# Kernel optimization log

Measured on AMD Instinct MI355X. Metric: run time of the kernel, lower is better.

The kernel has to match this reference:

```python
import jax, jax.numpy as jnp
import numpy as np

LORA_SCALE = 1.0 / 4.0  # alpha=1, rank=4
TAU_IOU = 0.1


def lora(x, W, A, B):
    # x @ W.T + (x @ A.T) @ B.T * scaling
    return x @ W.T + (x @ A.T) @ B.T * LORA_SCALE


def decode(h, Wd1, bd1, Wd2, bd2):
    # mask_decoder: Linear(embed,64) -> ReLU -> Linear(64,1)
    return (jax.nn.relu(h @ Wd1.T + bd1) @ Wd2.T + bd2)[..., 0]


def setup_inputs() -> dict:
    key = jax.random.key(0)
    ks = jax.random.split(key, 16)
    B, N, I, E, R = 2, 8192, 32, 128, 4
    s = lambda k, shape, f=0.05: jax.random.normal(k, shape, dtype=jnp.float32) * f
    return {
        "points": jax.random.normal(ks[0], (B, N, 3), dtype=jnp.float32),
        "pos_coords": jax.random.normal(ks[1], (B, I, 3), dtype=jnp.float32),
        "W1": s(ks[2], (64, 3), 0.3),
        "A1": s(ks[3], (R, 3), 0.3),
        "B1": s(ks[4], (64, R), 0.3),
        "W2": s(ks[5], (E, 64), 0.1),
        "A2": s(ks[6], (R, 64), 0.1),
        "B2": s(ks[7], (E, R), 0.1),
        "Wp": s(ks[8], (E, 3), 0.3),
        "bp": s(ks[9], (E,), 0.1),
        "Wd1": s(ks[10], (64, E), 0.1),
        "bd1": s(ks[11], (64,), 0.1),
        "Wd2": s(ks[12], (1, 64), 0.1),
        "bd2": s(ks[13], (1,), 0.1),
    }


def npc_neg_coords(initial_logits, pos_coords, key):
    # Vectorized replacement of the double python loop: for each (b,i),
    # uniformly sample one j with iou[b,i,j] >= tau (Gumbel-max trick);
    # if none, leave zeros.
    B, I, N = initial_logits.shape
    masks = (jax.nn.sigmoid(initial_logits) > 0.5).astype(initial_logits.dtype)  # [B,I,N]
    inter = jnp.einsum("bin,bjn->bij", masks, masks)
    m_sum = masks.sum(axis=2)  # [B,I]
    union = m_sum[:, :, None] + m_sum[:, None, :] - inter
    iou = inter / (union + 1e-6)
    iou = iou * (1.0 - jnp.eye(I, dtype=iou.dtype))  # zero diagonal
    cand = iou >= TAU_IOU  # [B,I,I]
    gumbel = -jnp.log(-jnp.log(jax.random.uniform(key, cand.shape, minval=1e-20, maxval=1.0)))
    scores = jnp.where(cand, gumbel, -jnp.inf)
    idx = jnp.argmax(scores, axis=-1)  # [B,I]
    valid = cand.any(axis=-1)  # [B,I]
    picked = jnp.take_along_axis(pos_coords, idx[..., None], axis=1)  # [B,I,3]
    return jnp.where(valid[..., None], picked, 0.0)


def reference(points, pos_coords, W1, A1, B1, W2, A2, B2, Wp, bp, Wd1, bd1, Wd2, bd2):
    # encoder: LoRA(3->64) -> ReLU -> LoRA(64->128)
    point_feats = lora(jax.nn.relu(lora(points, W1, A1, B1)), W2, A2, B2)  # [B,N,E]
    pos_embed = pos_coords @ Wp.T + bp  # [B,I,E]
    # [B,I,N,E] combined features
    initial_logits = decode(point_feats[:, None, :, :] + pos_embed[:, :, None, :], Wd1, bd1, Wd2, bd2)  # [B,I,N]
    neg_coords = npc_neg_coords(initial_logits, pos_coords, jax.random.key(42))
    neg_embed = neg_coords @ Wp.T + bp  # [B,I,E]
    refined_logits = decode(
        point_feats[:, None, :, :] + (pos_embed - neg_embed)[:, :, None, :], Wd1, bd1, Wd2, bd2
    )  # [B,I,N]
    return refined_logits, point_feats
```

## Files before the change

kernel.cpp:

```cpp
#include <hip/hip_runtime.h>

#define B_  2
#define N_  8192
#define I_  32
#define E_  128
#define H_  64
#define BN_ (B_*N_)
#define NW_ (N_/64)

typedef unsigned long long u64;

__device__ float g_pe  [B_*I_*E_];
__device__ float g_v1  [B_*I_*H_];
__device__ float g_v2  [B_*I_*H_];
__device__ float g_wd1t[E_*H_];
__device__ float g_u   [H_*BN_];
__device__ u64   g_masks[B_*I_*NW_];
__device__ int   g_inter[B_*I_*I_];

__device__ __forceinline__ unsigned rotl_(unsigned x, unsigned n){ return (x<<n)|(x>>(32u-n)); }

__device__ void threefry_42(unsigned x0, unsigned x1, unsigned* r0, unsigned* r1){
  const unsigned ks0 = 0u, ks1 = 42u, ks2 = 0x1BD11BDAu ^ 0u ^ 42u;
  x0 += ks0; x1 += ks1;
  x0+=x1; x1=rotl_(x1,13); x1^=x0;
  x0+=x1; x1=rotl_(x1,15); x1^=x0;
  x0+=x1; x1=rotl_(x1,26); x1^=x0;
  x0+=x1; x1=rotl_(x1, 6); x1^=x0;
  x0+=ks1; x1+=ks2+1u;
  x0+=x1; x1=rotl_(x1,17); x1^=x0;
  x0+=x1; x1=rotl_(x1,29); x1^=x0;
  x0+=x1; x1=rotl_(x1,16); x1^=x0;
  x0+=x1; x1=rotl_(x1,24); x1^=x0;
  x0+=ks2; x1+=ks0+2u;
  x0+=x1; x1=rotl_(x1,13); x1^=x0;
  x0+=x1; x1=rotl_(x1,15); x1^=x0;
  x0+=x1; x1=rotl_(x1,26); x1^=x0;
  x0+=x1; x1=rotl_(x1, 6); x1^=x0;
  x0+=ks0; x1+=ks1+3u;
  x0+=x1; x1=rotl_(x1,17); x1^=x0;
  x0+=x1; x1=rotl_(x1,29); x1^=x0;
  x0+=x1; x1=rotl_(x1,16); x1^=x0;
  x0+=x1; x1=rotl_(x1,24); x1^=x0;
  x0+=ks1; x1+=ks2+4u;
  x0+=x1; x1=rotl_(x1,13); x1^=x0;
  x0+=x1; x1=rotl_(x1,15); x1^=x0;
  x0+=x1; x1=rotl_(x1,26); x1^=x0;
  x0+=x1; x1=rotl_(x1, 6); x1^=x0;
  x0+=ks2; x1+=ks0+5u;
  *r0 = x0; *r1 = x1;
}

__device__ float jax_uniform_2048(int e){
  unsigned o0, o1;
  threefry_42(0u, (unsigned)e, &o0, &o1);
  unsigned bits = o0 ^ o1;
  float u = __uint_as_float((bits >> 9) | 0x3f800000u) - 1.0f;
  u = u + 1e-20f;
  return fmaxf(1e-20f, u);
}

__global__ void __launch_bounds__(256) prep_kernel(
    const float* __restrict__ pos_coords,
    const float* __restrict__ Wp, const float* __restrict__ bp,
    const float* __restrict__ Wd1,const float* __restrict__ bd1)
{
  __shared__ float t_l [E_*65];
  __shared__ float pe_l[E_];
  const int row = blockIdx.x;
  const int tid = threadIdx.x;

  for (int idx = tid; idx < H_*E_; idx += 256){
    int k = idx >> 7, e = idx & 127;
    t_l[e*65 + k] = Wd1[idx];
  }
  if (tid < E_){
    const int e = tid;
    float s = pos_coords[row*3+0] * Wp[e*3+0];
    s = fmaf(pos_coords[row*3+1], Wp[e*3+1], s);
    s = fmaf(pos_coords[row*3+2], Wp[e*3+2], s);
    const float pe = s + bp[e];
    g_pe[row*E_ + e] = pe;
    pe_l[e] = pe;
  }
  __syncthreads();

  if (row == 0){
    for (int idx = tid; idx < E_*H_; idx += 256){
      int e = idx >> 6, k = idx & 63;
      g_wd1t[idx] = t_l[e*65 + k];
    }
  }
  if (tid < H_){
    const int k = tid;
    float s = 0.f;
    for (int e = 0; e < 128; ++e)
      s = fmaf(pe_l[e], t_l[e*65 + k], s);
    g_v1[row*H_ + k] = s + bd1[k];
  }
}

__global__ void __launch_bounds__(512) enc_kernel(
    const float* __restrict__ points,
    const float* __restrict__ W1, const float* __restrict__ A1,
    const float* __restrict__ B1, const float* __restrict__ W2,
    const float* __restrict__ A2, const float* __restrict__ B2,
    const float* __restrict__ Wd2,const float* __restrict__ bd2,
    float* __restrict__ out_pf)
{
  __shared__ float pf_l[E_*65];
  __shared__ float u_l [64*65];
  const int tid  = threadIdx.x;
  const int w_u  = __builtin_amdgcn_readfirstlane(tid >> 6);
  const int lane = tid & 63;
  const int p0   = blockIdx.x * 64;
  const int p    = p0 + lane;
  const int b    = blockIdx.x >> 7;

  const float x0 = points[p*3+0];
  const float x1 = points[p*3+1];
  const float x2 = points[p*3+2];

  float a1[4];
  #pragma unroll
  for (int r = 0; r < 4; ++r){
    float s = x0 * A1[r*3+0];
    s = fmaf(x1, A1[r*3+1], s);
    s = fmaf(x2, A1[r*3+2], s);
    a1[r] = s;
  }
  float t1[64];
  #pragma unroll
  for (int k = 0; k < 64; ++k){
    float s = x0 * W1[k*3+0];
    s = fmaf(x1, W1[k*3+1], s);
    s = fmaf(x2, W1[k*3+2], s);
    float l = a1[0] * B1[k*4+0];
    l = fmaf(a1[1], B1[k*4+1], l);
    l = fmaf(a1[2], B1[k*4+2], l);
    l = fmaf(a1[3], B1[k*4+3], l);
    t1[k] = fmaxf(fmaf(0.25f, l, s), 0.0f);
  }
  float a2[4];
  #pragma unroll
  for (int r = 0; r < 4; ++r){
    float s = 0.f;
    #pragma unroll
    for (int j = 0; j < 64; ++j) s = fmaf(t1[j], A2[r*64+j], s);
    a2[r] = s;
  }

  const int e0 = w_u * 16;
  for (int ei = 0; ei < 16; ++ei){
    const int e = e0 + ei;
    float s1 = 0.f;
    #pragma unroll
    for (int j = 0; j < 64; ++j) s1 = fmaf(t1[j], W2[e*64+j], s1);
    float s2 = a2[0] * B2[e*4+0];
    s2 = fmaf(a2[1], B2[e*4+1], s2);
    s2 = fmaf(a2[2], B2[e*4+2], s2);
    s2 = fmaf(a2[3], B2[e*4+3], s2);
    pf_l[e*65 + lane] = fmaf(0.25f, s2, s1);
  }
  __syncthreads();

  const int kbase = w_u * 8;
  float uacc[8];
  #pragma unroll
  for (int kk = 0; kk < 8; ++kk) uacc[kk] = 0.f;
  for (int e = 0; e < 128; ++e){
    const float pf = pf_l[e*65 + lane];
    #pragma unroll
    for (int kk = 0; kk < 8; ++kk)
      uacc[kk] = fmaf(pf, g_wd1t[e*64 + kbase + kk], uacc[kk]);
  }
  #pragma unroll
  for (int kk = 0; kk < 8; ++kk){
    g_u[(size_t)(kbase + kk) * BN_ + p] = uacc[kk];
    u_l[lane*65 + kbase + kk] = uacc[kk];
  }
  __syncthreads();

  for (int idx = tid; idx < 64*E_; idx += 512){
    const int pt = idx >> 7, e = idx & 127;
    out_pf[(size_t)p0 * E_ + idx] = pf_l[e*65 + pt];
  }

  const float bd2v = bd2[0];
  float acc[4];
  #pragma unroll
  for (int ii = 0; ii < 4; ++ii) acc[ii] = 0.f;
  const int ibase = w_u * 4;
  const float* v = g_v1 + ((b * I_ + ibase) << 6);
  for (int k = 0; k < 64; ++k){
    const float wd2k = Wd2[k];
    const float uk = u_l[lane*65 + k];
    #pragma unroll
    for (int ii = 0; ii < 4; ++ii)
      acc[ii] = fmaf(wd2k, fmaxf(uk + v[ii*64 + k], 0.0f), acc[ii]);
  }
  #pragma unroll
  for (int ii = 0; ii < 4; ++ii){
    const int i = ibase + ii;
    u64 bal = __ballot(acc[ii] + bd2v > 0.0f);
    if (lane == 0) g_masks[(size_t)(b * I_ + i) * NW_ + (blockIdx.x & 127)] = bal;
  }
}

__global__ void __launch_bounds__(256) inter_kernel()
{
  const int r   = blockIdx.x;
  const int b   = r >> 5;
  const int tid = threadIdx.x;
  const int j   = tid >> 3;
  const int ws  = (tid & 7) * 16;
  const u64* mi = g_masks + (size_t)r * NW_;
  const u64* mj = g_masks + (size_t)(b*32 + j) * NW_;
  int s = 0;
  #pragma unroll
  for (int w = 0; w < 16; ++w)
    s += __popcll(mi[ws + w] & mj[ws + w]);
  s += __shfl_xor(s, 1, 64);
  s += __shfl_xor(s, 2, 64);
  s += __shfl_xor(s, 4, 64);
  if ((tid & 7) == 0) g_inter[r*32 + j] = s;
}

__global__ void __launch_bounds__(256) sample_kernel(
    const float* __restrict__ pos_coords,
    const float* __restrict__ Wp, const float* __restrict__ bp,
    const float* __restrict__ bd1)
{
  __shared__ int   inter_l[2048];
  __shared__ float delta_l[4*E_];
  __shared__ float nc_l[4][3];
  const int tid  = threadIdx.x;
  const int row0 = blockIdx.x * 4;

  for (int idx = tid; idx < 2048; idx += 256) inter_l[idx] = g_inter[idx];
  __syncthreads();

  if (tid < 4){
    const int row = row0 + tid;
    const int b = row >> 5;
    const int i = row & 31;
    const int msum_i = inter_l[(b << 10) + (i << 5) + i];
    float best = -INFINITY; int bestj = 0; bool any = false;
    for (int j = 0; j < 32; ++j){
      const int inter = inter_l[(b << 10) + (i << 5) + j];
      const int msum_j = inter_l[(b << 10) + (j << 5) + j];
      const int uni   = msum_i + msum_j - inter;
      const float iou = (float)inter / ((float)uni + 1e-6f);
      const bool cand = (j != i) && (iou >= 0.1f);
      if (cand){
        any = true;
        const float uu = jax_uniform_2048((row << 5) + j);
        const float g  = -logf(-logf(uu));
        if (g > best){ best = g; bestj = j; }
      }
    }
    nc_l[tid][0] = any ? pos_coords[(b*32 + bestj)*3 + 0] : 0.f;
    nc_l[tid][1] = any ? pos_coords[(b*32 + bestj)*3 + 1] : 0.f;
    nc_l[tid][2] = any ? pos_coords[(b*32 + bestj)*3 + 2] : 0.f;
  }
  __syncthreads();

  for (int idx = tid; idx < 4*E_; idx += 256){
    const int rl = idx >> 7, e = idx & 127;
    float ne = nc_l[rl][0] * Wp[e*3+0];
    ne = fmaf(nc_l[rl][1], Wp[e*3+1], ne);
    ne = fmaf(nc_l[rl][2], Wp[e*3+2], ne);
    ne = ne + bp[e];
    delta_l[idx] = g_pe[(row0 + rl)*E_ + e] - ne;
  }
  __syncthreads();

  {
    const int rl = tid >> 6, k = tid & 63;
    float s = 0.f;
    for (int e = 0; e < 128; ++e)
      s = fmaf(delta_l[rl*E_ + e], g_wd1t[e*64 + k], s);
    g_v2[(row0 + rl)*H_ + k] = s + bd1[k];
  }
}

__global__ void __launch_bounds__(256) dec_kernel(
    const float* __restrict__ Wd2, const float* __restrict__ bd2,
    float* __restrict__ out0)
{
  const int tid  = threadIdx.x;
  const int w_u  = __builtin_amdgcn_readfirstlane(tid >> 6);
  const int lane = tid & 63;
  const int bc   = blockIdx.x;
  const int b    = bc >> 8;
  const int nb   = (bc & 127) << 6;
  const int ih   = (bc >> 7) & 1;
  const int n    = nb + lane;
  const int p    = b * N_ + n;

  float u[64];
  #pragma unroll
  for (int k = 0; k < 64; ++k) u[k] = g_u[(size_t)k * BN_ + p];

  const float bd2v = bd2[0];
  float acc[4];
  #pragma unroll
  for (int ii = 0; ii < 4; ++ii) acc[ii] = 0.f;
  const int ibase = ih * 16 + w_u * 4;
  const float* v = g_v2 + ((b * I_ + ibase) << 6);
  for (int k = 0; k < 64; ++k){
    const float wd2k = Wd2[k];
    const float uk = u[k];
    #pragma unroll
    for (int ii = 0; ii < 4; ++ii)
      acc[ii] = fmaf(wd2k, fmaxf(uk + v[ii*64 + k], 0.0f), acc[ii]);
  }
  #pragma unroll
  for (int ii = 0; ii < 4; ++ii){
    const int i = ibase + ii;
    out0[(size_t)(b * I_ + i) * N_ + n] = acc[ii] + bd2v;
  }
}

extern "C" void kernel_launch(void* const* d_in, const int* in_sizes, int n_in,
                              void* d_out, int out_size, void* d_ws, size_t ws_size,
                              hipStream_t stream)
{
  (void)in_sizes; (void)n_in; (void)out_size; (void)d_ws; (void)ws_size;
  const float* points     = (const float*)d_in[0];
  const float* pos_coords = (const float*)d_in[1];
  const float* W1  = (const float*)d_in[2];
  const float* A1  = (const float*)d_in[3];
  const float* B1  = (const float*)d_in[4];
  const float* W2  = (const float*)d_in[5];
  const float* A2  = (const float*)d_in[6];
  const float* B2  = (const float*)d_in[7];
  const float* Wp  = (const float*)d_in[8];
  const float* bp  = (const float*)d_in[9];
  const float* Wd1 = (const float*)d_in[10];
  const float* bd1 = (const float*)d_in[11];
  const float* Wd2 = (const float*)d_in[12];
  const float* bd2 = (const float*)d_in[13];

  float* out0   = (float*)d_out;
  float* out_pf = out0 + (size_t)B_ * I_ * N_;

  prep_kernel<<<64, 256, 0, stream>>>(pos_coords, Wp, bp, Wd1, bd1);
  enc_kernel<<<256, 512, 0, stream>>>(points, W1, A1, B1, W2, A2, B2,
                                      Wd2, bd2, out_pf);
  inter_kernel<<<64, 256, 0, stream>>>();
  sample_kernel<<<16, 256, 0, stream>>>(pos_coords, Wp, bp, bd1);
  dec_kernel<<<512, 256, 0, stream>>>(Wd2, bd2, out0);
}
```

Before: 149.8 us.

## Double block size in encoder and decoder, stage u vectors through LDS

The encoder kernel goes from 512 to 1024 threads per block, so each wave computes half as many embedding channels, hidden units and instance masks. The decoder now launches 256 blocks of 1024 threads. Each block loads its 64-point u tile into shared memory once and shares it across all 32 instances, instead of every thread holding 64 registers loaded from global memory twice per point. The goal is more waves in flight and less redundant global reading of u, at the cost of larger blocks, an extra barrier and LDS reads in the inner loop.

```diff
diff --git a/kernel.cpp b/kernel.cpp
--- a/kernel.cpp
+++ b/kernel.cpp
@@ -100,7 +100,7 @@
   }
 }
 
-__global__ void __launch_bounds__(512) enc_kernel(
+__global__ void __launch_bounds__(1024) enc_kernel(
     const float* __restrict__ points,
     const float* __restrict__ W1, const float* __restrict__ A1,
     const float* __restrict__ B1, const float* __restrict__ W2,
@@ -150,8 +150,8 @@
     a2[r] = s;
   }
 
-  const int e0 = w_u * 16;
-  for (int ei = 0; ei < 16; ++ei){
+  const int e0 = w_u * 8;
+  for (int ei = 0; ei < 8; ++ei){
     const int e = e0 + ei;
     float s1 = 0.f;
     #pragma unroll
@@ -164,43 +164,41 @@
   }
   __syncthreads();
 
-  const int kbase = w_u * 8;
-  float uacc[8];
-  #pragma unroll
-  for (int kk = 0; kk < 8; ++kk) uacc[kk] = 0.f;
+  const int kbase = w_u * 4;
+  float uacc[4];
+  #pragma unroll
+  for (int kk = 0; kk < 4; ++kk) uacc[kk] = 0.f;
   for (int e = 0; e < 128; ++e){
     const float pf = pf_l[e*65 + lane];
     #pragma unroll
-    for (int kk = 0; kk < 8; ++kk)
+    for (int kk = 0; kk < 4; ++kk)
       uacc[kk] = fmaf(pf, g_wd1t[e*64 + kbase + kk], uacc[kk]);
   }
   #pragma unroll
-  for (int kk = 0; kk < 8; ++kk){
+  for (int kk = 0; kk < 4; ++kk){
     g_u[(size_t)(kbase + kk) * BN_ + p] = uacc[kk];
     u_l[lane*65 + kbase + kk] = uacc[kk];
   }
   __syncthreads();
 
-  for (int idx = tid; idx < 64*E_; idx += 512){
+  for (int idx = tid; idx < 64*E_; idx += 1024){
     const int pt = idx >> 7, e = idx & 127;
     out_pf[(size_t)p0 * E_ + idx] = pf_l[e*65 + pt];
   }
 
   const float bd2v = bd2[0];
-  float acc[4];
-  #pragma unroll
-  for (int ii = 0; ii < 4; ++ii) acc[ii] = 0.f;
-  const int ibase = w_u * 4;
+  float acc[2];
+  acc[0] = 0.f; acc[1] = 0.f;
+  const int ibase = w_u * 2;
   const float* v = g_v1 + ((b * I_ + ibase) << 6);
   for (int k = 0; k < 64; ++k){
     const float wd2k = Wd2[k];
     const float uk = u_l[lane*65 + k];
-    #pragma unroll
-    for (int ii = 0; ii < 4; ++ii)
-      acc[ii] = fmaf(wd2k, fmaxf(uk + v[ii*64 + k], 0.0f), acc[ii]);
-  }
-  #pragma unroll
-  for (int ii = 0; ii < 4; ++ii){
+    acc[0] = fmaf(wd2k, fmaxf(uk + v[k],      0.0f), acc[0]);
+    acc[1] = fmaf(wd2k, fmaxf(uk + v[64 + k], 0.0f), acc[1]);
+  }
+  #pragma unroll
+  for (int ii = 0; ii < 2; ++ii){
     const int i = ibase + ii;
     u64 bal = __ballot(acc[ii] + bd2v > 0.0f);
     if (lane == 0) g_masks[(size_t)(b * I_ + i) * NW_ + (blockIdx.x & 127)] = bal;
@@ -284,39 +282,38 @@
   }
 }
 
-__global__ void __launch_bounds__(256) dec_kernel(
+__global__ void __launch_bounds__(1024) dec_kernel(
     const float* __restrict__ Wd2, const float* __restrict__ bd2,
     float* __restrict__ out0)
 {
+  __shared__ float u_l[64*65];
   const int tid  = threadIdx.x;
   const int w_u  = __builtin_amdgcn_readfirstlane(tid >> 6);
   const int lane = tid & 63;
   const int bc   = blockIdx.x;
-  const int b    = bc >> 8;
+  const int b    = bc >> 7;
   const int nb   = (bc & 127) << 6;
-  const int ih   = (bc >> 7) & 1;
   const int n    = nb + lane;
-  const int p    = b * N_ + n;
-
-  float u[64];
-  #pragma unroll
-  for (int k = 0; k < 64; ++k) u[k] = g_u[(size_t)k * BN_ + p];
+
+  for (int idx = tid; idx < 64*64; idx += 1024){
+    const int k = idx >> 6, pl = idx & 63;
+    u_l[pl*65 + k] = g_u[(size_t)k * BN_ + b * N_ + nb + pl];
+  }
+  __syncthreads();
 
   const float bd2v = bd2[0];
-  float acc[4];
-  #pragma unroll
-  for (int ii = 0; ii < 4; ++ii) acc[ii] = 0.f;
-  const int ibase = ih * 16 + w_u * 4;
+  float acc[2];
+  acc[0] = 0.f; acc[1] = 0.f;
+  const int ibase = w_u * 2;
   const float* v = g_v2 + ((b * I_ + ibase) << 6);
   for (int k = 0; k < 64; ++k){
     const float wd2k = Wd2[k];
-    const float uk = u[k];
-    #pragma unroll
-    for (int ii = 0; ii < 4; ++ii)
-      acc[ii] = fmaf(wd2k, fmaxf(uk + v[ii*64 + k], 0.0f), acc[ii]);
-  }
-  #pragma unroll
-  for (int ii = 0; ii < 4; ++ii){
+    const float uk = u_l[lane*65 + k];
+    acc[0] = fmaf(wd2k, fmaxf(uk + v[k],      0.0f), acc[0]);
+    acc[1] = fmaf(wd2k, fmaxf(uk + v[64 + k], 0.0f), acc[1]);
+  }
+  #pragma unroll
+  for (int ii = 0; ii < 2; ++ii){
     const int i = ibase + ii;
     out0[(size_t)(b * I_ + i) * N_ + n] = acc[ii] + bd2v;
   }
@@ -346,9 +343,9 @@
   float* out_pf = out0 + (size_t)B_ * I_ * N_;
 
   prep_kernel<<<64, 256, 0, stream>>>(pos_coords, Wp, bp, Wd1, bd1);
-  enc_kernel<<<256, 512, 0, stream>>>(points, W1, A1, B1, W2, A2, B2,
-                                      Wd2, bd2, out_pf);
+  enc_kernel<<<256, 1024, 0, stream>>>(points, W1, A1, B1, W2, A2, B2,
+                                       Wd2, bd2, out_pf);
   inter_kernel<<<64, 256, 0, stream>>>();
   sample_kernel<<<16, 256, 0, stream>>>(pos_coords, Wp, bp, bd1);
-  dec_kernel<<<512, 256, 0, stream>>>(Wd2, bd2, out0);
-}
+  dec_kernel<<<256, 1024, 0, stream>>>(Wd2, bd2, out0);
+}
```

Result: slower. 183.8 us (+22.7%).
